# Performance work log

Hardware: AMD Instinct MI355X
Metric: run time of the kernel (lower is better)

The kernel has to match this reference:

```python
import jax, jax.numpy as jnp
import numpy as np

B = 64          # graphs per batch
NP = 512        # nodes per graph (equal-sized graphs)
N = B * NP      # total nodes
E = 1_048_576   # total edges (avg degree 32)
F_IN, H, K, OUT = 16, 128, 2, 2
BN_EPS = 1e-5
EPS = 1e-15


def setup_inputs() -> dict:
    key = jax.random.key(0)
    ks = jax.random.split(key, 12)
    node_feature = jax.random.normal(ks[0], (N, F_IN), jnp.float32)
    # edges constrained to stay within each graph of NP nodes
    g = jax.random.randint(ks[1], (E,), 0, B)
    src = g * NP + jax.random.randint(ks[2], (E,), 0, NP)
    dst = g * NP + jax.random.randint(ks[3], (E,), 0, NP)
    edge_index = jnp.stack([src, dst]).astype(jnp.int32)
    edge_feature = jax.random.uniform(ks[4], (E, 1), jnp.float32)
    batch = (jnp.arange(N, dtype=jnp.int32) // NP)

    def lin(k, i, o):
        return (jax.random.normal(k, (i, o), jnp.float32) / np.sqrt(i)).astype(jnp.float32)

    params = dict(
        W_pre=lin(ks[5], F_IN, H), b_pre=jnp.zeros((H,), jnp.float32),
        W1_rel=lin(ks[6], H, H), b1_rel=jnp.zeros((H,), jnp.float32), W1_root=lin(ks[7], H, H),
        g1=jnp.ones((H,), jnp.float32), be1=jnp.zeros((H,), jnp.float32),
        W2_rel=lin(ks[8], H, H), b2_rel=jnp.zeros((H,), jnp.float32), W2_root=lin(ks[9], H, H),
        g2=jnp.ones((H,), jnp.float32), be2=jnp.zeros((H,), jnp.float32),
        W_pool=lin(ks[10], H, K), b_pool=jnp.zeros((K,), jnp.float32),
        W_post=lin(ks[11], 2 * H, OUT), b_post=jnp.zeros((OUT,), jnp.float32),
    )
    return dict(node_feature=node_feature, edge_index=edge_index,
                edge_feature=edge_feature, batch=batch, **params)


def _graph_conv(x, src, dst, ew, W_rel, b_rel, W_root):
    # PyG GraphConv: out = lin_rel(sum_{j->i} w_e * x_j) + lin_root(x_i)
    msg = x[src] * ew                       # [E, H] gather + scale
    agg = jnp.zeros_like(x).at[dst].add(msg)  # scatter-add to targets
    return agg @ W_rel + b_rel + x @ W_root


def _bn(x, g, b):
    # BatchNorm1d in training mode: batch statistics over nodes (biased var)
    mu = x.mean(0)
    var = jnp.mean((x - mu) ** 2, axis=0)
    return (x - mu) * jax.lax.rsqrt(var + BN_EPS) * g + b


def reference(node_feature, edge_index, edge_feature, batch,
              W_pre, b_pre, W1_rel, b1_rel, W1_root, g1, be1,
              W2_rel, b2_rel, W2_root, g2, be2,
              W_pool, b_pool, W_post, b_post):
    src, dst = edge_index[0], edge_index[1]
    x = node_feature @ W_pre + b_pre
    x = jax.nn.relu(_bn(_graph_conv(x, src, dst, edge_feature, W1_rel, b1_rel, W1_root), g1, be1))
    x = jax.nn.relu(_bn(_graph_conv(x, src, dst, edge_feature, W2_rel, b2_rel, W2_root), g2, be2))
    # dropout p=0.0 -> identity

    # to_dense_batch: equal-sized sorted graphs -> reshape; mask is all-ones
    xd = x.reshape(B, NP, H)
    # to_dense_adj: scatter edge weights into [B, NP, NP]
    gid, ls, ld = src // NP, src % NP, dst % NP
    adj = jnp.zeros((B, NP, NP), jnp.float32).at[gid, ls, ld].add(edge_feature[:, 0])

    # dense_mincut_pool
    s = jax.nn.softmax(xd @ W_pool + b_pool, axis=-1)          # [B, NP, K]
    out = jnp.einsum('bnk,bnh->bkh', s, xd)                     # [B, K, H]
    out_adj = jnp.einsum('bnk,bnm,bml->bkl', s, adj, s)         # [B, K, K]

    mincut_num = jnp.trace(out_adj, axis1=1, axis2=2)
    d_flat = adj.sum(-1)                                        # [B, NP]
    den_mat = jnp.einsum('bnk,bn,bnl->bkl', s, d_flat, s)
    mincut_den = jnp.trace(den_mat, axis1=1, axis2=2)
    mc_loss = jnp.mean(-(mincut_num / mincut_den))

    ss = jnp.einsum('bnk,bnl->bkl', s, s)                       # [B, K, K]
    ss_n = jnp.linalg.norm(ss, axis=(-2, -1), keepdims=True)
    i_s = jnp.eye(K, dtype=ss.dtype)
    o_loss = jnp.mean(jnp.linalg.norm(ss / ss_n - i_s / jnp.sqrt(jnp.float32(K)), axis=(-2, -1)))

    h = jax.nn.relu(out).reshape(B, K * H)
    logits = h @ W_post + b_post
    return (logits, mc_loss, o_loss)
```

## Files before the change

kernel.cpp:

```cpp
#include <hip/hip_runtime.h>

#define NN 32768
#define NP 512
#define NB 64
#define NE 1048576
#define FIN 16
#define H 128
#define BN_EPS 1e-5f
#define EPB 4096
#define NBLK (NE / EPB)
#define CAPH 8704
#define NSH 16

typedef unsigned int u32;
typedef unsigned short u16;
typedef __attribute__((ext_vector_type(8))) short bf16x8;
typedef __attribute__((ext_vector_type(4))) float f32x4;

__device__ __forceinline__ u16 f2bf(float f) {
    u32 u = __float_as_uint(f);
    return (u16)((u + 0x7fffu + ((u >> 16) & 1u)) >> 16);
}
__device__ __forceinline__ float bfLo(u32 p) { return __uint_as_float(p << 16); }
__device__ __forceinline__ float bfHi(u32 p) { return __uint_as_float(p & 0xffff0000u); }
__device__ __forceinline__ float b2f(u16 v) { return __uint_as_float((u32)v << 16); }

static constexpr size_t SZ_HALF   = (size_t)NN * H * 2;
static constexpr size_t OFF_X     = 0;
static constexpr size_t OFF_AGG   = OFF_X + SZ_HALF;
static constexpr size_t OFF_TMP   = OFF_AGG;
static constexpr size_t OFF_SORT  = OFF_AGG + SZ_HALF;
static constexpr size_t OFF_OFFS  = OFF_SORT + (size_t)NE * 8;
static constexpr size_t OFF_HISTG = OFF_OFFS + ((size_t)NN + 128) * 4;
static constexpr size_t OFF_STARTG= OFF_HISTG + (size_t)NBLK * NB * 4;
static constexpr size_t OFF_GBASE = OFF_STARTG + (size_t)NBLK * NB * 4;
static constexpr size_t OFF_WT1   = OFF_GBASE + 512;
static constexpr size_t OFF_WT2   = OFF_WT1 + (size_t)H * 2 * H * 2;
static constexpr size_t OFF_S     = OFF_WT2 + (size_t)H * 2 * H * 2;
static constexpr size_t OFF_SCSH  = OFF_S + (size_t)NN * 2 * 4;
static constexpr size_t OFF_GST   = OFF_SCSH + 4 * H * 4;
static constexpr size_t OFF_ZERO  = OFF_GST + 1024;
static constexpr size_t OFF_NUM   = OFF_ZERO;
static constexpr size_t OFF_DEN   = OFF_NUM + 256;
static constexpr size_t OFF_BN    = OFF_DEN + 256;
static constexpr size_t SZ_BNL    = (size_t)NSH * 2 * H * 4;
static constexpr size_t OFF_POOL  = OFF_BN + 2 * SZ_BNL;
static constexpr size_t ZERO_BYTES= (OFF_POOL + (size_t)NB * 2 * H * 4) - OFF_ZERO;


__global__ void k_pre(const float* __restrict__ nf, const float* __restrict__ Wp,
                      const float* __restrict__ bp, u16* __restrict__ x0) {
    __shared__ float sW[FIN * H];
    __shared__ float sNF[8 * FIN];
    int tid = threadIdx.x;
    for (int i = tid; i < FIN * H; i += 128) sW[i] = Wp[i];
    int n0 = blockIdx.x * 8;
    sNF[tid] = nf[n0 * FIN + tid];
    __syncthreads();
    float b = bp[tid];
    #pragma unroll
    for (int r = 0; r < 8; ++r) {
        float acc = b;
        #pragma unroll
        for (int f = 0; f < FIN; ++f) acc += sNF[r * FIN + f] * sW[f * H + tid];
        x0[(size_t)(n0 + r) * H + tid] = f2bf(acc);
    }
}

__global__ void k_wprep(const float* __restrict__ Wrel, const float* __restrict__ Wroot,
                        u16* __restrict__ WT) {
    int i = blockIdx.x * 256 + threadIdx.x;
    int c = i >> 8, k = i & 255;
    float v = (k < H) ? Wrel[k * H + c] : Wroot[(k - H) * H + c];
    WT[c * 256 + k] = f2bf(v);
}

__global__ __launch_bounds__(256) void k_hist(const int* __restrict__ src,
                                              int* __restrict__ histG) {
    __shared__ int h[NB];
    int t = threadIdx.x, bid = blockIdx.x;
    if (t < NB) h[t] = 0;
    __syncthreads();
    int ebase = bid * EPB;
    #pragma unroll
    for (int i = 0; i < EPB / 256; ++i) {
        int s = src[ebase + i * 256 + t];
        atomicAdd(&h[s >> 9], 1);
    }
    __syncthreads();
    if (t < NB) histG[bid * NB + t] = h[t];
}

__global__ __launch_bounds__(1024) void k_scanG(const int* __restrict__ histG,
                                                int* __restrict__ startG,
                                                int* __restrict__ gbase) {
    __shared__ int csum[16][64];
    __shared__ int gpre[64];
    int t = threadIdx.x;
    int g = t & 63, c = t >> 6;
    int vals[16];
    int s = 0;
    #pragma unroll
    for (int i = 0; i < 16; ++i) {
        vals[i] = histG[(c * 16 + i) * NB + g];
        s += vals[i];
    }
    csum[c][g] = s;
    __syncthreads();
    int pre = 0;
    for (int i = 0; i < c; ++i) pre += csum[i][g];
    if (c == 0) {
        int tot = 0;
        #pragma unroll
        for (int i = 0; i < 16; ++i) tot += csum[i][g];
        int x = tot;
        #pragma unroll
        for (int o = 1; o < 64; o <<= 1) {
            int y = __shfl_up(x, o);
            if (g >= o) x += y;
        }
        gpre[g] = x - tot;
        gbase[g] = x - tot;
        if (g == 63) gbase[64] = x;
    }
    __syncthreads();
    int run = gpre[g] + pre;
    #pragma unroll
    for (int i = 0; i < 16; ++i) {
        startG[(c * 16 + i) * NB + g] = run;
        run += vals[i];
    }
}

__global__ __launch_bounds__(256) void k_scatterA(
        const int* __restrict__ src, const int* __restrict__ dst,
        const float* __restrict__ ew, const int* __restrict__ histG,
        const int* __restrict__ startG, int2* __restrict__ tmp) {
    __shared__ int lstart[NB + 1];
    __shared__ int cursor[NB];
    __shared__ int gdst[NB];
    __shared__ int2 buf[EPB];
    int t = threadIdx.x, bid = blockIdx.x;
    if (t < NB) {
        int c = histG[bid * NB + t];
        int x = c;
        #pragma unroll
        for (int o = 1; o < 64; o <<= 1) {
            int y = __shfl_up(x, o);
            if (t >= o) x += y;
        }
        lstart[t] = x - c;
        cursor[t] = x - c;
        gdst[t] = startG[bid * NB + t];
        if (t == 63) lstart[NB] = x;
    }
    __syncthreads();
    int ebase = bid * EPB;
    #pragma unroll
    for (int i = 0; i < EPB / 256; ++i) {
        int e = ebase + i * 256 + t;
        int s = src[e], d = dst[e];
        float w = ew[e];
        int g = s >> 9;
        int meta = (s & 511) | ((d & 511) << 9);
        int p = atomicAdd(&cursor[g], 1);
        buf[p] = make_int2(meta, __float_as_int(w));
    }
    __syncthreads();
    for (int g = 0; g < NB; ++g) {
        int lo = lstart[g], hi = lstart[g + 1];
        int base = gdst[g];
        for (int i = lo + t; i < hi; i += 256) tmp[base + (i - lo)] = buf[i];
    }
}

__global__ __launch_bounds__(512) void k_sortB(
        const int2* __restrict__ tmp, const int* __restrict__ gbase,
        int2* __restrict__ sorted, int* __restrict__ offs) {
    __shared__ int hist[NP];
    __shared__ int start[NP + 1];
    __shared__ int cursor[NP / 2];
    __shared__ int perm[CAPH];
    int t = threadIdx.x;
    int g = blockIdx.x >> 1, half = blockIdx.x & 1;
    int gbeg = gbase[g], gend = gbase[g + 1];
    int cnt = gend - gbeg;
    if (t < NP) hist[t] = 0;
    __syncthreads();
    for (int i = t; i < cnt; i += 512) {
        int meta = tmp[gbeg + i].x;
        atomicAdd(&hist[(meta >> 9) & 511], 1);
    }
    __syncthreads();
    if (t < NP) start[t] = hist[t];
    __syncthreads();
    for (int o = 1; o < NP; o <<= 1) {
        int v = 0;
        if (t >= o && t < NP) v = start[t - o];
        __syncthreads();
        if (t < NP) start[t] += v;
        __syncthreads();
    }
    if (t < NP) start[t] -= hist[t];
    if (t == 0) start[NP] = cnt;
    __syncthreads();
    int h0 = half * 256;
    if (t < 256) {
        int n = h0 + t;
        offs[g * NP + n] = gbeg + start[n];
        cursor[t] = start[n];
    }
    if (blockIdx.x == 0 && t == 0) offs[NN] = NE;
    __syncthreads();
    int ha = start[h0];
    int hb = half ? cnt : start[256];
    for (int i = t; i < cnt; i += 512) {
        int meta = tmp[gbeg + i].x;
        int d = (meta >> 9) & 511;
        if ((d >> 8) == half) {
            int p = atomicAdd(&cursor[d - h0], 1);
            perm[p - ha] = i;
        }
    }
    __syncthreads();
    for (int o = ha + t; o < hb; o += 512) {
        sorted[gbeg + o] = tmp[gbeg + perm[o - ha]];
    }
}

__global__ __launch_bounds__(256) void k_agg(const u16* __restrict__ x,
        const int* __restrict__ offs, const int2* __restrict__ rec,
        u16* __restrict__ agg) {
    int wv = threadIdx.x >> 6, lane = threadIdx.x & 63;
    int b = blockIdx.x;
    int swz = (b & 7) * (NN / 8 / 4) + (b >> 3);
    int node = swz * 4 + wv;
    int sbase = node & ~(NP - 1);
    const u16* xg = x + (size_t)sbase * H;
    int beg = offs[node], end = offs[node + 1];
    float a0 = 0.f, a1 = 0.f;
    int j = beg;
    for (; j + 4 <= end; j += 4) {
        int2 r0 = rec[j], r1 = rec[j + 1], r2 = rec[j + 2], r3 = rec[j + 3];
        u32 p0 = *(const u32*)(xg + (size_t)(r0.x & 511) * H + 2 * lane);
        u32 p1 = *(const u32*)(xg + (size_t)(r1.x & 511) * H + 2 * lane);
        u32 p2 = *(const u32*)(xg + (size_t)(r2.x & 511) * H + 2 * lane);
        u32 p3 = *(const u32*)(xg + (size_t)(r3.x & 511) * H + 2 * lane);
        float w0 = __int_as_float(r0.y), w1 = __int_as_float(r1.y);
        float w2 = __int_as_float(r2.y), w3 = __int_as_float(r3.y);
        a0 += w0 * bfLo(p0); a1 += w0 * bfHi(p0);
        a0 += w1 * bfLo(p1); a1 += w1 * bfHi(p1);
        a0 += w2 * bfLo(p2); a1 += w2 * bfHi(p2);
        a0 += w3 * bfLo(p3); a1 += w3 * bfHi(p3);
    }
    for (; j < end; ++j) {
        int2 r = rec[j];
        u32 p = *(const u32*)(xg + (size_t)(r.x & 511) * H + 2 * lane);
        float w = __int_as_float(r.y);
        a0 += w * bfLo(p); a1 += w * bfHi(p);
    }
    u32 packed = (u32)f2bf(a0) | ((u32)f2bf(a1) << 16);
    *(u32*)(agg + (size_t)node * H + 2 * lane) = packed;
}

__global__ __launch_bounds__(256) void k_gemm(
        const u16* __restrict__ Amat, const u16* Xmat,
        const u16* __restrict__ WT, const float* __restrict__ brel,
        u16* Y, float* __restrict__ bn_base) {
    __shared__ u16 sWT[128][264];
    __shared__ float colS[128], colQ[128];
    int tid = threadIdx.x;
    int w = tid >> 6, lane = tid & 63;
    int lr = lane & 15, lg = lane >> 4;
    int row0 = blockIdx.x * 64;
    int myrow = row0 + w * 16 + lr;

    bf16x8 af[8];
    const u16* pa = Amat + (size_t)myrow * H + lg * 8;
    const u16* px = Xmat + (size_t)myrow * H + lg * 8;
    #pragma unroll
    for (int kt = 0; kt < 4; ++kt) af[kt] = *(const bf16x8*)(pa + kt * 32);
    #pragma unroll
    for (int kt = 0; kt < 4; ++kt) af[4 + kt] = *(const bf16x8*)(px + kt * 32);

    for (int i = tid; i < 128 * 32; i += 256) {
        int r = i >> 5, c = i & 31;
        *(uint4*)&sWT[r][c * 8] = *(const uint4*)(WT + r * 256 + c * 8);
    }
    if (tid < 128) { colS[tid] = 0.f; colQ[tid] = 0.f; }
    __syncthreads();

    f32x4 acc[8];
    #pragma unroll
    for (int nt = 0; nt < 8; ++nt) acc[nt] = (f32x4){0.f, 0.f, 0.f, 0.f};

    #pragma unroll
    for (int kt = 0; kt < 8; ++kt) {
        #pragma unroll
        for (int nt = 0; nt < 8; ++nt) {
            bf16x8 bf = *(const bf16x8*)&sWT[nt * 16 + lr][kt * 32 + lg * 8];
            acc[nt] = __builtin_amdgcn_mfma_f32_16x16x32_bf16(af[kt], bf, acc[nt], 0, 0, 0);
        }
    }

    float cs[8], cq[8];
    #pragma unroll
    for (int nt = 0; nt < 8; ++nt) {
        int col = nt * 16 + lr;
        float bias = brel[col];
        float s = 0.f, q = 0.f;
        #pragma unroll
        for (int j = 0; j < 4; ++j) {
            float v = acc[nt][j] + bias;
            int row = row0 + w * 16 + lg * 4 + j;
            Y[(size_t)row * H + col] = f2bf(v);
            s += v; q += v * v;
        }
        cs[nt] = s; cq[nt] = q;
    }
    #pragma unroll
    for (int nt = 0; nt < 8; ++nt) {
        cs[nt] += __shfl_xor(cs[nt], 16); cs[nt] += __shfl_xor(cs[nt], 32);
        cq[nt] += __shfl_xor(cq[nt], 16); cq[nt] += __shfl_xor(cq[nt], 32);
    }
    if (lg == 0) {
        #pragma unroll
        for (int nt = 0; nt < 8; ++nt) {
            atomicAdd(&colS[nt * 16 + lr], cs[nt]);
            atomicAdd(&colQ[nt * 16 + lr], cq[nt]);
        }
    }
    __syncthreads();
    if (tid < 128) {
        int sh = blockIdx.x & (NSH - 1);
        atomicAdd(&bn_base[(sh * 2 + 0) * H + tid], colS[tid]);
        atomicAdd(&bn_base[(sh * 2 + 1) * H + tid], colQ[tid]);
    }
}

__global__ void k_bnfinal(const float* __restrict__ bn_base, const float* __restrict__ g,
                          const float* __restrict__ be, float* __restrict__ sc_sh) {
    int t = threadIdx.x;
    float su = 0.f, sq = 0.f;
    #pragma unroll
    for (int sh = 0; sh < NSH; ++sh) {
        su += bn_base[(sh * 2 + 0) * H + t];
        sq += bn_base[(sh * 2 + 1) * H + t];
    }
    float mu = su * (1.f / NN);
    float var = sq * (1.f / NN) - mu * mu;
    float sc = rsqrtf(var + BN_EPS) * g[t];
    sc_sh[t] = sc;
    sc_sh[H + t] = be[t] - mu * sc;
}

__global__ void k_bnrelu(u16* __restrict__ y, const float* __restrict__ sc_sh) {
    int idx = blockIdx.x * 256 + threadIdx.x;
    int c = (idx & 15) * 8;
    uint4 u = ((const uint4*)y)[idx];
    u32 uu[4] = {u.x, u.y, u.z, u.w};
    u32 ro[4];
    #pragma unroll
    for (int p = 0; p < 4; ++p) {
        float v0 = fmaxf(fmaf(bfLo(uu[p]), sc_sh[c + 2 * p], sc_sh[H + c + 2 * p]), 0.f);
        float v1 = fmaxf(fmaf(bfHi(uu[p]), sc_sh[c + 2 * p + 1], sc_sh[H + c + 2 * p + 1]), 0.f);
        ro[p] = (u32)f2bf(v0) | ((u32)f2bf(v1) << 16);
    }
    uint4 o; o.x = ro[0]; o.y = ro[1]; o.z = ro[2]; o.w = ro[3];
    ((uint4*)y)[idx] = o;
}

__global__ void k_bnrelu_s(u16* __restrict__ y, const float* __restrict__ sc_sh,
                           const float* __restrict__ Wp, const float* __restrict__ bp,
                           float* __restrict__ s) {
    int tid = threadIdx.x;
    int idx = blockIdx.x * 256 + tid;
    int c = (idx & 15) * 8;
    uint4 u = ((const uint4*)y)[idx];
    u32 uu[4] = {u.x, u.y, u.z, u.w};
    u32 ro[4];
    float z0 = 0.f, z1 = 0.f;
    #pragma unroll
    for (int p = 0; p < 4; ++p) {
        float v0 = fmaxf(fmaf(bfLo(uu[p]), sc_sh[c + 2 * p], sc_sh[H + c + 2 * p]), 0.f);
        float v1 = fmaxf(fmaf(bfHi(uu[p]), sc_sh[c + 2 * p + 1], sc_sh[H + c + 2 * p + 1]), 0.f);
        ro[p] = (u32)f2bf(v0) | ((u32)f2bf(v1) << 16);
        z0 += v0 * Wp[(c + 2 * p) * 2] + v1 * Wp[(c + 2 * p + 1) * 2];
        z1 += v0 * Wp[(c + 2 * p) * 2 + 1] + v1 * Wp[(c + 2 * p + 1) * 2 + 1];
    }
    uint4 o; o.x = ro[0]; o.y = ro[1]; o.z = ro[2]; o.w = ro[3];
    ((uint4*)y)[idx] = o;
    #pragma unroll
    for (int off = 8; off; off >>= 1) {
        z0 += __shfl_down(z0, off);
        z1 += __shfl_down(z1, off);
    }
    if ((tid & 15) == 0) {
        int row = idx >> 4;
        z0 += bp[0]; z1 += bp[1];
        float m = fmaxf(z0, z1);
        float e0 = expf(z0 - m), e1 = expf(z1 - m);
        float inv = 1.f / (e0 + e1);
        s[row * 2] = e0 * inv;
        s[row * 2 + 1] = e1 * inv;
    }
}

__global__ void k_pool_out(const u16* __restrict__ x, const float* __restrict__ s,
                           float* __restrict__ pool) {
    int b = blockIdx.x & 63, chunk = blockIdx.x >> 6;
    int h = threadIdx.x;
    float a0 = 0.f, a1 = 0.f;
    int n0 = b * NP + chunk * 64;
    for (int i = 0; i < 64; ++i) {
        float2 sv = ((const float2*)s)[n0 + i];
        float xv = b2f(x[(size_t)(n0 + i) * H + h]);
        a0 += sv.x * xv;
        a1 += sv.y * xv;
    }
    atomicAdd(&pool[(b * 2 + 0) * H + h], a0);
    atomicAdd(&pool[(b * 2 + 1) * H + h], a1);
}

__global__ __launch_bounds__(256) void k_edge_stats(
        const int2* __restrict__ sorted, const int* __restrict__ gbase,
        const float* __restrict__ s, float* __restrict__ num, float* __restrict__ den,
        float* __restrict__ gst) {
    __shared__ float2 sl[NP];
    __shared__ float ln[4], ld2[4];
    int t = threadIdx.x;
    int g = blockIdx.x >> 2, q = blockIdx.x & 3;
    int gbeg = gbase[g], gend = gbase[g + 1];
    for (int i = t; i < NP; i += 256) sl[i] = ((const float2*)s)[g * NP + i];
    __syncthreads();
    float an = 0.f, ad = 0.f;
    int cnt = gend - gbeg;
    int q0 = gbeg + (cnt * q) / 4, q1 = gbeg + (cnt * (q + 1)) / 4;
    for (int i = q0 + t; i < q1; i += 256) {
        int2 r = sorted[i];
        float w = __int_as_float(r.y);
        float2 ss = sl[r.x & 511];
        float2 sd = sl[(r.x >> 9) & 511];
        an += w * (ss.x * sd.x + ss.y * sd.y);
        ad += w * (ss.x * ss.x + ss.y * ss.y);
    }
    for (int o = 32; o; o >>= 1) { an += __shfl_down(an, o); ad += __shfl_down(ad, o); }
    if ((t & 63) == 0) { ln[t >> 6] = an; ld2[t >> 6] = ad; }
    __syncthreads();
    if (t == 0) {
        atomicAdd(&num[g], ln[0] + ln[1] + ln[2] + ln[3]);
        atomicAdd(&den[g], ld2[0] + ld2[1] + ld2[2] + ld2[3]);
    }
    if (q == 0) {
        float p00 = 0.f, p01 = 0.f, p11 = 0.f;
        for (int i = t; i < NP; i += 256) {
            float2 sv = sl[i];
            p00 += sv.x * sv.x;
            p01 += sv.x * sv.y;
            p11 += sv.y * sv.y;
        }
        for (int o = 32; o; o >>= 1) {
            p00 += __shfl_down(p00, o);
            p01 += __shfl_down(p01, o);
            p11 += __shfl_down(p11, o);
        }
        __shared__ float tp[3][4];
        if ((t & 63) == 0) {
            int w = t >> 6;
            tp[0][w] = p00; tp[1][w] = p01; tp[2][w] = p11;
        }
        __syncthreads();
        if (t == 0) {
            gst[g] = tp[0][0] + tp[0][1] + tp[0][2] + tp[0][3];
            gst[NB + g] = tp[1][0] + tp[1][1] + tp[1][2] + tp[1][3];
            gst[2 * NB + g] = tp[2][0] + tp[2][1] + tp[2][2] + tp[2][3];
        }
    }
}

__global__ void k_logits_losses(const float* __restrict__ pool, const float* __restrict__ Wpost,
                                const float* __restrict__ bpost, const float* __restrict__ num,
                                const float* __restrict__ den, const float* __restrict__ gst,
                                float* __restrict__ out) {
    int t = threadIdx.x;
    if (blockIdx.x < 64) {
        int b = blockIdx.x;
        float v = pool[b * 256 + t];
        v = v > 0.f ? v : 0.f;
        float p0 = v * Wpost[t * 2], p1 = v * Wpost[t * 2 + 1];
        for (int o = 32; o; o >>= 1) { p0 += __shfl_down(p0, o); p1 += __shfl_down(p1, o); }
        __shared__ float t0[4], t1[4];
        if ((t & 63) == 0) { t0[t >> 6] = p0; t1[t >> 6] = p1; }
        __syncthreads();
        if (t == 0) {
            out[b * 2] = t0[0] + t0[1] + t0[2] + t0[3] + bpost[0];
            out[b * 2 + 1] = t1[0] + t1[1] + t1[2] + t1[3] + bpost[1];
        }
    } else if (t < 64) {
        float s00 = gst[t], s01 = gst[NB + t], s11 = gst[2 * NB + t];
        float mc = -(num[t] / den[t]);
        float nrm = sqrtf(s00 * s00 + 2.f * s01 * s01 + s11 * s11);
        const float a = 0.70710678118654752440f;
        float d00 = s00 / nrm - a, d01 = s01 / nrm, d11 = s11 / nrm - a;
        float ol = sqrtf(d00 * d00 + 2.f * d01 * d01 + d11 * d11);
        for (int o = 32; o; o >>= 1) { mc += __shfl_down(mc, o); ol += __shfl_down(ol, o); }
        if (t == 0) {
            out[NB * 2] = mc * (1.f / NB);
            out[NB * 2 + 1] = ol * (1.f / NB);
        }
    }
}

extern "C" void kernel_launch(void* const* d_in, const int* in_sizes, int n_in,
                              void* d_out, int out_size, void* d_ws, size_t ws_size,
                              hipStream_t stream) {
    const float* nf     = (const float*)d_in[0];
    const int*   ei     = (const int*)d_in[1];
    const float* ew     = (const float*)d_in[2];
    const float* W_pre  = (const float*)d_in[4];
    const float* b_pre  = (const float*)d_in[5];
    const float* W1_rel = (const float*)d_in[6];
    const float* b1_rel = (const float*)d_in[7];
    const float* W1_root= (const float*)d_in[8];
    const float* g1     = (const float*)d_in[9];
    const float* be1    = (const float*)d_in[10];
    const float* W2_rel = (const float*)d_in[11];
    const float* b2_rel = (const float*)d_in[12];
    const float* W2_root= (const float*)d_in[13];
    const float* g2     = (const float*)d_in[14];
    const float* be2    = (const float*)d_in[15];
    const float* W_pool = (const float*)d_in[16];
    const float* b_pool = (const float*)d_in[17];
    const float* W_post = (const float*)d_in[18];
    const float* b_post = (const float*)d_in[19];

    char* ws = (char*)d_ws;
    u16*   bufX   = (u16*)(ws + OFF_X);
    u16*   bufAgg = (u16*)(ws + OFF_AGG);
    int2*  tmp    = (int2*)(ws + OFF_TMP);
    int2*  sorted = (int2*)(ws + OFF_SORT);
    int*   offs   = (int*)(ws + OFF_OFFS);
    int*   histG  = (int*)(ws + OFF_HISTG);
    int*   startG = (int*)(ws + OFF_STARTG);
    int*   gbase  = (int*)(ws + OFF_GBASE);
    u16*   WT1    = (u16*)(ws + OFF_WT1);
    u16*   WT2    = (u16*)(ws + OFF_WT2);
    float* sarr   = (float*)(ws + OFF_S);
    float* scsh   = (float*)(ws + OFF_SCSH);
    float* gst    = (float*)(ws + OFF_GST);
    float* numA   = (float*)(ws + OFF_NUM);
    float* denA   = (float*)(ws + OFF_DEN);
    float* bn     = (float*)(ws + OFF_BN);
    float* pool   = (float*)(ws + OFF_POOL);
    float* outF   = (float*)d_out;

    const int* srcA = ei;
    const int* dstA = ei + NE;
    float* bn1 = bn;
    float* bn2 = (float*)(ws + OFF_BN + SZ_BNL);

    hipMemsetAsync(ws + OFF_ZERO, 0, ZERO_BYTES, stream);

    k_pre<<<NN / 8, 128, 0, stream>>>(nf, W_pre, b_pre, bufX);
    k_wprep<<<(H * 2 * H) / 256, 256, 0, stream>>>(W1_rel, W1_root, WT1);
    k_wprep<<<(H * 2 * H) / 256, 256, 0, stream>>>(W2_rel, W2_root, WT2);
    k_hist<<<NBLK, 256, 0, stream>>>(srcA, histG);
    k_scanG<<<1, 1024, 0, stream>>>(histG, startG, gbase);
    k_scatterA<<<NBLK, 256, 0, stream>>>(srcA, dstA, ew, histG, startG, tmp);
    k_sortB<<<2 * NB, 512, 0, stream>>>(tmp, gbase, sorted, offs);

    k_agg<<<NN / 4, 256, 0, stream>>>(bufX, offs, sorted, bufAgg);
    k_gemm<<<NN / 64, 256, 0, stream>>>(bufAgg, bufX, WT1, b1_rel, bufX, bn1);
    k_bnfinal<<<1, H, 0, stream>>>(bn1, g1, be1, scsh);
    k_bnrelu<<<(NN * H / 8) / 256, 256, 0, stream>>>(bufX, scsh);

    k_agg<<<NN / 4, 256, 0, stream>>>(bufX, offs, sorted, bufAgg);
    k_gemm<<<NN / 64, 256, 0, stream>>>(bufAgg, bufX, WT2, b2_rel, bufX, bn2);
    k_bnfinal<<<1, H, 0, stream>>>(bn2, g2, be2, scsh + 2 * H);
    k_bnrelu_s<<<(NN * H / 8) / 256, 256, 0, stream>>>(bufX, scsh + 2 * H,
                                                       W_pool, b_pool, sarr);

    k_pool_out<<<8 * NB, 128, 0, stream>>>(bufX, sarr, pool);
    k_edge_stats<<<4 * NB, 256, 0, stream>>>(sorted, gbase, sarr, numA, denA, gst);
    k_logits_losses<<<NB + 1, 256, 0, stream>>>(pool, W_post, b_post, numA, denA, gst, outF);
}
```

Before: 297.5 us.

## Merge small kernels to cut launch count and speed up scans

Four prep kernels (pre-linear, two weight transposes, histogram) become one launch that dispatches on block index. The BN finalize step is folded into each bnrelu kernel, which now recomputes the scale and shift per block and handles four vectors per thread. Pool and edge-stats run in a single launch. The sortB prefix scan switches from a barrier-heavy Hillis-Steele loop to a wavefront shuffle scan, and the scatterA copy-out becomes one flat loop with a binary search instead of looping over the 64 groups. The aim is fewer launches and fewer barriers, paid for by redundant BN-stat reads in every block and divergent block roles inside the merged kernels.

```diff
diff --git a/kernel.cpp b/kernel.cpp
--- a/kernel.cpp
+++ b/kernel.cpp
@@ -37,8 +37,7 @@
 static constexpr size_t OFF_WT1   = OFF_GBASE + 512;
 static constexpr size_t OFF_WT2   = OFF_WT1 + (size_t)H * 2 * H * 2;
 static constexpr size_t OFF_S     = OFF_WT2 + (size_t)H * 2 * H * 2;
-static constexpr size_t OFF_SCSH  = OFF_S + (size_t)NN * 2 * 4;
-static constexpr size_t OFF_GST   = OFF_SCSH + 4 * H * 4;
+static constexpr size_t OFF_GST   = OFF_S + (size_t)NN * 2 * 4;
 static constexpr size_t OFF_ZERO  = OFF_GST + 1024;
 static constexpr size_t OFF_NUM   = OFF_ZERO;
 static constexpr size_t OFF_DEN   = OFF_NUM + 256;
@@ -48,47 +47,54 @@
 static constexpr size_t ZERO_BYTES= (OFF_POOL + (size_t)NB * 2 * H * 4) - OFF_ZERO;
 
 
-__global__ void k_pre(const float* __restrict__ nf, const float* __restrict__ Wp,
-                      const float* __restrict__ bp, u16* __restrict__ x0) {
-    __shared__ float sW[FIN * H];
-    __shared__ float sNF[8 * FIN];
-    int tid = threadIdx.x;
-    for (int i = tid; i < FIN * H; i += 128) sW[i] = Wp[i];
-    int n0 = blockIdx.x * 8;
-    sNF[tid] = nf[n0 * FIN + tid];
-    __syncthreads();
-    float b = bp[tid];
-    #pragma unroll
-    for (int r = 0; r < 8; ++r) {
-        float acc = b;
-        #pragma unroll
-        for (int f = 0; f < FIN; ++f) acc += sNF[r * FIN + f] * sW[f * H + tid];
-        x0[(size_t)(n0 + r) * H + tid] = f2bf(acc);
-    }
-}
-
-__global__ void k_wprep(const float* __restrict__ Wrel, const float* __restrict__ Wroot,
-                        u16* __restrict__ WT) {
-    int i = blockIdx.x * 256 + threadIdx.x;
-    int c = i >> 8, k = i & 255;
-    float v = (k < H) ? Wrel[k * H + c] : Wroot[(k - H) * H + c];
-    WT[c * 256 + k] = f2bf(v);
-}
-
-__global__ __launch_bounds__(256) void k_hist(const int* __restrict__ src,
-                                              int* __restrict__ histG) {
-    __shared__ int h[NB];
+__global__ __launch_bounds__(256) void k_prep(
+        const float* __restrict__ nf, const float* __restrict__ Wp,
+        const float* __restrict__ bp,
+        const float* __restrict__ W1_rel, const float* __restrict__ W1_root,
+        const float* __restrict__ W2_rel, const float* __restrict__ W2_root,
+        const int* __restrict__ src,
+        u16* __restrict__ x0, u16* __restrict__ WT1, u16* __restrict__ WT2,
+        int* __restrict__ histG) {
     int t = threadIdx.x, bid = blockIdx.x;
-    if (t < NB) h[t] = 0;
-    __syncthreads();
-    int ebase = bid * EPB;
-    #pragma unroll
-    for (int i = 0; i < EPB / 256; ++i) {
-        int s = src[ebase + i * 256 + t];
-        atomicAdd(&h[s >> 9], 1);
-    }
-    __syncthreads();
-    if (t < NB) histG[bid * NB + t] = h[t];
+    if (bid < 2048) {
+        __shared__ float sW[FIN * H];
+        __shared__ float sNF[16 * FIN];
+        for (int i = t; i < FIN * H; i += 256) sW[i] = Wp[i];
+        int n0 = bid * 16;
+        sNF[t] = nf[n0 * FIN + t];
+        __syncthreads();
+        int col = t & 127, half = t >> 7;
+        float b = bp[col];
+        #pragma unroll
+        for (int r = 0; r < 8; ++r) {
+            int rr = half * 8 + r;
+            float acc = b;
+            #pragma unroll
+            for (int f = 0; f < FIN; ++f) acc += sNF[rr * FIN + f] * sW[f * H + col];
+            x0[(size_t)(n0 + rr) * H + col] = f2bf(acc);
+        }
+    } else if (bid < 2304) {
+        int base = bid - 2048;
+        const float* __restrict__ Wrel = (base < 128) ? W1_rel : W2_rel;
+        const float* __restrict__ Wroot = (base < 128) ? W1_root : W2_root;
+        u16* WT = (base < 128) ? WT1 : WT2;
+        int i = (base & 127) * 256 + t;
+        int c = i >> 8, k = i & 255;
+        float v = (k < H) ? Wrel[k * H + c] : Wroot[(k - H) * H + c];
+        WT[c * 256 + k] = f2bf(v);
+    } else {
+        __shared__ int h[NB];
+        if (t < NB) h[t] = 0;
+        __syncthreads();
+        int ebase = (bid - 2304) * EPB;
+        #pragma unroll
+        for (int i = 0; i < EPB / 256; ++i) {
+            int s = src[ebase + i * 256 + t];
+            atomicAdd(&h[s >> 9], 1);
+        }
+        __syncthreads();
+        if (t < NB) histG[(bid - 2304) * NB + t] = h[t];
+    }
 }
 
 __global__ __launch_bounds__(1024) void k_scanG(const int* __restrict__ histG,
@@ -167,10 +173,12 @@
         buf[p] = make_int2(meta, __float_as_int(w));
     }
     __syncthreads();
-    for (int g = 0; g < NB; ++g) {
-        int lo = lstart[g], hi = lstart[g + 1];
-        int base = gdst[g];
-        for (int i = lo + t; i < hi; i += 256) tmp[base + (i - lo)] = buf[i];
+    for (int i = t; i < EPB; i += 256) {
+        int lo = 0;
+        #pragma unroll
+        for (int stp = 32; stp; stp >>= 1)
+            if (lstart[lo + stp] <= i) lo += stp;
+        tmp[gdst[lo] + (i - lstart[lo])] = buf[i];
     }
 }
 
@@ -180,29 +188,34 @@
     __shared__ int hist[NP];
     __shared__ int start[NP + 1];
     __shared__ int cursor[NP / 2];
+    __shared__ int wsum[8];
     __shared__ int perm[CAPH];
     int t = threadIdx.x;
+    int lane = t & 63, wv = t >> 6;
     int g = blockIdx.x >> 1, half = blockIdx.x & 1;
     int gbeg = gbase[g], gend = gbase[g + 1];
     int cnt = gend - gbeg;
-    if (t < NP) hist[t] = 0;
+    hist[t] = 0;
     __syncthreads();
     for (int i = t; i < cnt; i += 512) {
         int meta = tmp[gbeg + i].x;
         atomicAdd(&hist[(meta >> 9) & 511], 1);
     }
     __syncthreads();
-    if (t < NP) start[t] = hist[t];
-    __syncthreads();
-    for (int o = 1; o < NP; o <<= 1) {
-        int v = 0;
-        if (t >= o && t < NP) v = start[t - o];
-        __syncthreads();
-        if (t < NP) start[t] += v;
-        __syncthreads();
-    }
-    if (t < NP) start[t] -= hist[t];
-    if (t == 0) start[NP] = cnt;
+    int c = hist[t];
+    int x = c;
+    #pragma unroll
+    for (int o = 1; o < 64; o <<= 1) {
+        int y = __shfl_up(x, o);
+        if (lane >= o) x += y;
+    }
+    if (lane == 63) wsum[wv] = x;
+    __syncthreads();
+    int off = 0;
+    #pragma unroll
+    for (int i = 0; i < 8; ++i) off += (i < wv) ? wsum[i] : 0;
+    start[t] = off + x - c;
+    if (t == 511) start[NP] = off + x;
     __syncthreads();
     int h0 = half * 256;
     if (t < 256) {
@@ -338,142 +351,167 @@
     }
 }
 
-__global__ void k_bnfinal(const float* __restrict__ bn_base, const float* __restrict__ g,
-                          const float* __restrict__ be, float* __restrict__ sc_sh) {
+__global__ __launch_bounds__(256) void k_bnrelu(u16* __restrict__ y,
+        const float* __restrict__ bn_base, const float* __restrict__ g,
+        const float* __restrict__ be) {
+    __shared__ float scL[H], shL[H];
     int t = threadIdx.x;
-    float su = 0.f, sq = 0.f;
-    #pragma unroll
-    for (int sh = 0; sh < NSH; ++sh) {
-        su += bn_base[(sh * 2 + 0) * H + t];
-        sq += bn_base[(sh * 2 + 1) * H + t];
-    }
-    float mu = su * (1.f / NN);
-    float var = sq * (1.f / NN) - mu * mu;
-    float sc = rsqrtf(var + BN_EPS) * g[t];
-    sc_sh[t] = sc;
-    sc_sh[H + t] = be[t] - mu * sc;
-}
-
-__global__ void k_bnrelu(u16* __restrict__ y, const float* __restrict__ sc_sh) {
-    int idx = blockIdx.x * 256 + threadIdx.x;
-    int c = (idx & 15) * 8;
-    uint4 u = ((const uint4*)y)[idx];
-    u32 uu[4] = {u.x, u.y, u.z, u.w};
-    u32 ro[4];
-    #pragma unroll
-    for (int p = 0; p < 4; ++p) {
-        float v0 = fmaxf(fmaf(bfLo(uu[p]), sc_sh[c + 2 * p], sc_sh[H + c + 2 * p]), 0.f);
-        float v1 = fmaxf(fmaf(bfHi(uu[p]), sc_sh[c + 2 * p + 1], sc_sh[H + c + 2 * p + 1]), 0.f);
-        ro[p] = (u32)f2bf(v0) | ((u32)f2bf(v1) << 16);
-    }
-    uint4 o; o.x = ro[0]; o.y = ro[1]; o.z = ro[2]; o.w = ro[3];
-    ((uint4*)y)[idx] = o;
-}
-
-__global__ void k_bnrelu_s(u16* __restrict__ y, const float* __restrict__ sc_sh,
-                           const float* __restrict__ Wp, const float* __restrict__ bp,
-                           float* __restrict__ s) {
-    int tid = threadIdx.x;
-    int idx = blockIdx.x * 256 + tid;
-    int c = (idx & 15) * 8;
-    uint4 u = ((const uint4*)y)[idx];
-    u32 uu[4] = {u.x, u.y, u.z, u.w};
-    u32 ro[4];
-    float z0 = 0.f, z1 = 0.f;
-    #pragma unroll
-    for (int p = 0; p < 4; ++p) {
-        float v0 = fmaxf(fmaf(bfLo(uu[p]), sc_sh[c + 2 * p], sc_sh[H + c + 2 * p]), 0.f);
-        float v1 = fmaxf(fmaf(bfHi(uu[p]), sc_sh[c + 2 * p + 1], sc_sh[H + c + 2 * p + 1]), 0.f);
-        ro[p] = (u32)f2bf(v0) | ((u32)f2bf(v1) << 16);
-        z0 += v0 * Wp[(c + 2 * p) * 2] + v1 * Wp[(c + 2 * p + 1) * 2];
-        z1 += v0 * Wp[(c + 2 * p) * 2 + 1] + v1 * Wp[(c + 2 * p + 1) * 2 + 1];
-    }
-    uint4 o; o.x = ro[0]; o.y = ro[1]; o.z = ro[2]; o.w = ro[3];
-    ((uint4*)y)[idx] = o;
-    #pragma unroll
-    for (int off = 8; off; off >>= 1) {
-        z0 += __shfl_down(z0, off);
-        z1 += __shfl_down(z1, off);
-    }
-    if ((tid & 15) == 0) {
-        int row = idx >> 4;
-        z0 += bp[0]; z1 += bp[1];
-        float m = fmaxf(z0, z1);
-        float e0 = expf(z0 - m), e1 = expf(z1 - m);
-        float inv = 1.f / (e0 + e1);
-        s[row * 2] = e0 * inv;
-        s[row * 2 + 1] = e1 * inv;
-    }
-}
-
-__global__ void k_pool_out(const u16* __restrict__ x, const float* __restrict__ s,
-                           float* __restrict__ pool) {
-    int b = blockIdx.x & 63, chunk = blockIdx.x >> 6;
-    int h = threadIdx.x;
-    float a0 = 0.f, a1 = 0.f;
-    int n0 = b * NP + chunk * 64;
-    for (int i = 0; i < 64; ++i) {
-        float2 sv = ((const float2*)s)[n0 + i];
-        float xv = b2f(x[(size_t)(n0 + i) * H + h]);
-        a0 += sv.x * xv;
-        a1 += sv.y * xv;
-    }
-    atomicAdd(&pool[(b * 2 + 0) * H + h], a0);
-    atomicAdd(&pool[(b * 2 + 1) * H + h], a1);
-}
-
-__global__ __launch_bounds__(256) void k_edge_stats(
+    if (t < H) {
+        float su = 0.f, sq = 0.f;
+        #pragma unroll
+        for (int sh = 0; sh < NSH; ++sh) {
+            su += bn_base[(sh * 2 + 0) * H + t];
+            sq += bn_base[(sh * 2 + 1) * H + t];
+        }
+        float mu = su * (1.f / NN);
+        float var = sq * (1.f / NN) - mu * mu;
+        float sc = rsqrtf(var + BN_EPS) * g[t];
+        scL[t] = sc;
+        shL[t] = be[t] - mu * sc;
+    }
+    __syncthreads();
+    #pragma unroll
+    for (int it = 0; it < 4; ++it) {
+        int idx = blockIdx.x * 1024 + it * 256 + t;
+        int c = (idx & 15) * 8;
+        uint4 u = ((const uint4*)y)[idx];
+        u32 uu[4] = {u.x, u.y, u.z, u.w};
+        u32 ro[4];
+        #pragma unroll
+        for (int p = 0; p < 4; ++p) {
+            float v0 = fmaxf(fmaf(bfLo(uu[p]), scL[c + 2 * p], shL[c + 2 * p]), 0.f);
+            float v1 = fmaxf(fmaf(bfHi(uu[p]), scL[c + 2 * p + 1], shL[c + 2 * p + 1]), 0.f);
+            ro[p] = (u32)f2bf(v0) | ((u32)f2bf(v1) << 16);
+        }
+        uint4 o; o.x = ro[0]; o.y = ro[1]; o.z = ro[2]; o.w = ro[3];
+        ((uint4*)y)[idx] = o;
+    }
+}
+
+__global__ __launch_bounds__(256) void k_bnrelu_s(u16* __restrict__ y,
+        const float* __restrict__ bn_base, const float* __restrict__ g,
+        const float* __restrict__ be, const float* __restrict__ Wp,
+        const float* __restrict__ bp, float* __restrict__ s) {
+    __shared__ float scL[H], shL[H];
+    int t = threadIdx.x;
+    if (t < H) {
+        float su = 0.f, sq = 0.f;
+        #pragma unroll
+        for (int sh = 0; sh < NSH; ++sh) {
+            su += bn_base[(sh * 2 + 0) * H + t];
+            sq += bn_base[(sh * 2 + 1) * H + t];
+        }
+        float mu = su * (1.f / NN);
+        float var = sq * (1.f / NN) - mu * mu;
+        float sc = rsqrtf(var + BN_EPS) * g[t];
+        scL[t] = sc;
+        shL[t] = be[t] - mu * sc;
+    }
+    __syncthreads();
+    #pragma unroll
+    for (int it = 0; it < 4; ++it) {
+        int idx = blockIdx.x * 1024 + it * 256 + t;
+        int c = (idx & 15) * 8;
+        uint4 u = ((const uint4*)y)[idx];
+        u32 uu[4] = {u.x, u.y, u.z, u.w};
+        u32 ro[4];
+        float z0 = 0.f, z1 = 0.f;
+        #pragma unroll
+        for (int p = 0; p < 4; ++p) {
+            float v0 = fmaxf(fmaf(bfLo(uu[p]), scL[c + 2 * p], shL[c + 2 * p]), 0.f);
+            float v1 = fmaxf(fmaf(bfHi(uu[p]), scL[c + 2 * p + 1], shL[c + 2 * p + 1]), 0.f);
+            ro[p] = (u32)f2bf(v0) | ((u32)f2bf(v1) << 16);
+            z0 += v0 * Wp[(c + 2 * p) * 2] + v1 * Wp[(c + 2 * p + 1) * 2];
+            z1 += v0 * Wp[(c + 2 * p) * 2 + 1] + v1 * Wp[(c + 2 * p + 1) * 2 + 1];
+        }
+        uint4 o; o.x = ro[0]; o.y = ro[1]; o.z = ro[2]; o.w = ro[3];
+        ((uint4*)y)[idx] = o;
+        #pragma unroll
+        for (int off = 8; off; off >>= 1) {
+            z0 += __shfl_down(z0, off);
+            z1 += __shfl_down(z1, off);
+        }
+        if ((t & 15) == 0) {
+            int row = idx >> 4;
+            z0 += bp[0]; z1 += bp[1];
+            float m = fmaxf(z0, z1);
+            float e0 = expf(z0 - m), e1 = expf(z1 - m);
+            float inv = 1.f / (e0 + e1);
+            s[row * 2] = e0 * inv;
+            s[row * 2 + 1] = e1 * inv;
+        }
+    }
+}
+
+__global__ __launch_bounds__(256) void k_pool_edge(
+        const u16* __restrict__ x, const float* __restrict__ s,
         const int2* __restrict__ sorted, const int* __restrict__ gbase,
-        const float* __restrict__ s, float* __restrict__ num, float* __restrict__ den,
-        float* __restrict__ gst) {
-    __shared__ float2 sl[NP];
-    __shared__ float ln[4], ld2[4];
-    int t = threadIdx.x;
-    int g = blockIdx.x >> 2, q = blockIdx.x & 3;
-    int gbeg = gbase[g], gend = gbase[g + 1];
-    for (int i = t; i < NP; i += 256) sl[i] = ((const float2*)s)[g * NP + i];
-    __syncthreads();
-    float an = 0.f, ad = 0.f;
-    int cnt = gend - gbeg;
-    int q0 = gbeg + (cnt * q) / 4, q1 = gbeg + (cnt * (q + 1)) / 4;
-    for (int i = q0 + t; i < q1; i += 256) {
-        int2 r = sorted[i];
-        float w = __int_as_float(r.y);
-        float2 ss = sl[r.x & 511];
-        float2 sd = sl[(r.x >> 9) & 511];
-        an += w * (ss.x * sd.x + ss.y * sd.y);
-        ad += w * (ss.x * ss.x + ss.y * ss.y);
-    }
-    for (int o = 32; o; o >>= 1) { an += __shfl_down(an, o); ad += __shfl_down(ad, o); }
-    if ((t & 63) == 0) { ln[t >> 6] = an; ld2[t >> 6] = ad; }
-    __syncthreads();
-    if (t == 0) {
-        atomicAdd(&num[g], ln[0] + ln[1] + ln[2] + ln[3]);
-        atomicAdd(&den[g], ld2[0] + ld2[1] + ld2[2] + ld2[3]);
-    }
-    if (q == 0) {
-        float p00 = 0.f, p01 = 0.f, p11 = 0.f;
-        for (int i = t; i < NP; i += 256) {
-            float2 sv = sl[i];
-            p00 += sv.x * sv.x;
-            p01 += sv.x * sv.y;
-            p11 += sv.y * sv.y;
-        }
-        for (int o = 32; o; o >>= 1) {
-            p00 += __shfl_down(p00, o);
-            p01 += __shfl_down(p01, o);
-            p11 += __shfl_down(p11, o);
-        }
-        __shared__ float tp[3][4];
-        if ((t & 63) == 0) {
-            int w = t >> 6;
-            tp[0][w] = p00; tp[1][w] = p01; tp[2][w] = p11;
-        }
+        float* __restrict__ pool, float* __restrict__ num,
+        float* __restrict__ den, float* __restrict__ gst) {
+    int bid = blockIdx.x, t = threadIdx.x;
+    if (bid < 256) {
+        int b = bid & 63, chunk = bid >> 6;
+        int h = t & 127, sub = t >> 7;
+        int n0 = b * NP + chunk * 128 + sub * 64;
+        float a0 = 0.f, a1 = 0.f;
+        for (int i = 0; i < 64; ++i) {
+            float2 sv = ((const float2*)s)[n0 + i];
+            float xv = b2f(x[(size_t)(n0 + i) * H + h]);
+            a0 += sv.x * xv;
+            a1 += sv.y * xv;
+        }
+        atomicAdd(&pool[(b * 2 + 0) * H + h], a0);
+        atomicAdd(&pool[(b * 2 + 1) * H + h], a1);
+    } else {
+        __shared__ float2 sl[NP];
+        __shared__ float ln[4], ld2[4];
+        int ebid = bid - 256;
+        int g = ebid >> 2, q = ebid & 3;
+        int gbeg = gbase[g], gend = gbase[g + 1];
+        for (int i = t; i < NP; i += 256) sl[i] = ((const float2*)s)[g * NP + i];
+        __syncthreads();
+        float an = 0.f, ad = 0.f;
+        int cnt = gend - gbeg;
+        int q0 = gbeg + (cnt * q) / 4, q1 = gbeg + (cnt * (q + 1)) / 4;
+        for (int i = q0 + t; i < q1; i += 256) {
+            int2 r = sorted[i];
+            float w = __int_as_float(r.y);
+            float2 ss = sl[r.x & 511];
+            float2 sd = sl[(r.x >> 9) & 511];
+            an += w * (ss.x * sd.x + ss.y * sd.y);
+            ad += w * (ss.x * ss.x + ss.y * ss.y);
+        }
+        for (int o = 32; o; o >>= 1) { an += __shfl_down(an, o); ad += __shfl_down(ad, o); }
+        if ((t & 63) == 0) { ln[t >> 6] = an; ld2[t >> 6] = ad; }
         __syncthreads();
         if (t == 0) {
-            gst[g] = tp[0][0] + tp[0][1] + tp[0][2] + tp[0][3];
-            gst[NB + g] = tp[1][0] + tp[1][1] + tp[1][2] + tp[1][3];
-            gst[2 * NB + g] = tp[2][0] + tp[2][1] + tp[2][2] + tp[2][3];
+            atomicAdd(&num[g], ln[0] + ln[1] + ln[2] + ln[3]);
+            atomicAdd(&den[g], ld2[0] + ld2[1] + ld2[2] + ld2[3]);
+        }
+        if (q == 0) {
+            float p00 = 0.f, p01 = 0.f, p11 = 0.f;
+            for (int i = t; i < NP; i += 256) {
+                float2 sv = sl[i];
+                p00 += sv.x * sv.x;
+                p01 += sv.x * sv.y;
+                p11 += sv.y * sv.y;
+            }
+            for (int o = 32; o; o >>= 1) {
+                p00 += __shfl_down(p00, o);
+                p01 += __shfl_down(p01, o);
+                p11 += __shfl_down(p11, o);
+            }
+            __shared__ float tp[3][4];
+            if ((t & 63) == 0) {
+                int w = t >> 6;
+                tp[0][w] = p00; tp[1][w] = p01; tp[2][w] = p11;
+            }
+            __syncthreads();
+            if (t == 0) {
+                gst[g] = tp[0][0] + tp[0][1] + tp[0][2] + tp[0][3];
+                gst[NB + g] = tp[1][0] + tp[1][1] + tp[1][2] + tp[1][3];
+                gst[2 * NB + g] = tp[2][0] + tp[2][1] + tp[2][2] + tp[2][3];
+            }
         }
     }
 }
@@ -546,7 +584,6 @@
     u16*   WT1    = (u16*)(ws + OFF_WT1);
     u16*   WT2    = (u16*)(ws + OFF_WT2);
     float* sarr   = (float*)(ws + OFF_S);
-    float* scsh   = (float*)(ws + OFF_SCSH);
     float* gst    = (float*)(ws + OFF_GST);
     float* numA   = (float*)(ws + OFF_NUM);
     float* denA   = (float*)(ws + OFF_DEN);
@@ -561,26 +598,20 @@
 
     hipMemsetAsync(ws + OFF_ZERO, 0, ZERO_BYTES, stream);
 
-    k_pre<<<NN / 8, 128, 0, stream>>>(nf, W_pre, b_pre, bufX);
-    k_wprep<<<(H * 2 * H) / 256, 256, 0, stream>>>(W1_rel, W1_root, WT1);
-    k_wprep<<<(H * 2 * H) / 256, 256, 0, stream>>>(W2_rel, W2_root, WT2);
-    k_hist<<<NBLK, 256, 0, stream>>>(srcA, histG);
+    k_prep<<<2560, 256, 0, stream>>>(nf, W_pre, b_pre, W1_rel, W1_root,
+                                     W2_rel, W2_root, srcA, bufX, WT1, WT2, histG);
     k_scanG<<<1, 1024, 0, stream>>>(histG, startG, gbase);
     k_scatterA<<<NBLK, 256, 0, stream>>>(srcA, dstA, ew, histG, startG, tmp);
     k_sortB<<<2 * NB, 512, 0, stream>>>(tmp, gbase, sorted, offs);
 
     k_agg<<<NN / 4, 256, 0, stream>>>(bufX, offs, sorted, bufAgg);
     k_gemm<<<NN / 64, 256, 0, stream>>>(bufAgg, bufX, WT1, b1_rel, bufX, bn1);
-    k_bnfinal<<<1, H, 0, stream>>>(bn1, g1, be1, scsh);
-    k_bnrelu<<<(NN * H / 8) / 256, 256, 0, stream>>>(bufX, scsh);
+    k_bnrelu<<<512, 256, 0, stream>>>(bufX, bn1, g1, be1);
 
     k_agg<<<NN / 4, 256, 0, stream>>>(bufX, offs, sorted, bufAgg);
     k_gemm<<<NN / 64, 256, 0, stream>>>(bufAgg, bufX, WT2, b2_rel, bufX, bn2);
-    k_bnfinal<<<1, H, 0, stream>>>(bn2, g2, be2, scsh + 2 * H);
-    k_bnrelu_s<<<(NN * H / 8) / 256, 256, 0, stream>>>(bufX, scsh + 2 * H,
-                                                       W_pool, b_pool, sarr);
-
-    k_pool_out<<<8 * NB, 128, 0, stream>>>(bufX, sarr, pool);
-    k_edge_stats<<<4 * NB, 256, 0, stream>>>(sorted, gbase, sarr, numA, denA, gst);
+    k_bnrelu_s<<<512, 256, 0, stream>>>(bufX, bn2, g2, be2, W_pool, b_pool, sarr);
+
+    k_pool_edge<<<512, 256, 0, stream>>>(bufX, sarr, sorted, gbase, pool, numA, denA, gst);
     k_logits_losses<<<NB + 1, 256, 0, stream>>>(pool, W_post, b_post, numA, denA, gst, outF);
 }
```

Measured after the change: 275.8 us. 7.3% less time.
